# Performance work log

Measured on AMD Instinct MI355X. Metric: run time of the kernel, lower is better.

The kernel has to match this reference:

```python
import jax, jax.numpy as jnp
import numpy as np

N = 50000       # nodes
E = 800000      # edges (avg degree 16)
IN = 256        # input features
HEADS = 4
D = 32          # per-head dim (hidden_channels/heads = 128/4)
HID = HEADS * D # 128
OUT = 64        # out_channels, last layer has 1 head
SLOPE = 0.2     # DGL GATConv LeakyReLU negative slope


def setup_inputs() -> dict:
    key = jax.random.key(0)
    ks = jax.random.split(key, 11)
    s = 0.05
    return {
        "x": jax.random.normal(ks[0], (N, IN), jnp.float32),
        "W1": jax.random.normal(ks[1], (IN, HID), jnp.float32) * s,
        "al1": jax.random.normal(ks[2], (HEADS, D), jnp.float32) * s,
        "ar1": jax.random.normal(ks[3], (HEADS, D), jnp.float32) * s,
        "b1": jnp.zeros((HID,), jnp.float32),
        "W2": jax.random.normal(ks[4], (HID, OUT), jnp.float32) * s,
        "al2": jax.random.normal(ks[5], (1, OUT), jnp.float32) * s,
        "ar2": jax.random.normal(ks[6], (1, OUT), jnp.float32) * s,
        "b2": jnp.zeros((OUT,), jnp.float32),
        "src": jax.random.randint(ks[7], (E,), 0, N),
        "dst": jax.random.randint(ks[8], (E,), 0, N),
    }


def gat_conv(h, W, al, ar, b, src, dst, heads, d):
    # h: [N, F_in]; projects, computes edge attention, edge-softmax over dst,
    # scatter-reduce aggregation. Matches dglnn.GATConv (bias, no residual).
    feat = (h @ W).reshape(-1, heads, d)              # [N, H, D]
    el = jnp.einsum('nhd,hd->nh', feat, al)           # [N, H]
    er = jnp.einsum('nhd,hd->nh', feat, ar)           # [N, H]
    e = jax.nn.leaky_relu(el[src] + er[dst], SLOPE)   # [E, H] edge scores
    # edge softmax over incoming edges of each dst node
    m = jax.ops.segment_max(e, dst, num_segments=N)   # [N, H]
    ee = jnp.exp(e - m[dst])                          # [E, H]
    z = jax.ops.segment_sum(ee, dst, num_segments=N)  # [N, H]
    a = ee / z[dst]                                   # [E, H]
    msg = feat[src] * a[:, :, None]                   # [E, H, D] gather + weight
    out = jax.ops.segment_sum(msg, dst, num_segments=N)  # [N, H, D]
    return out + b.reshape(heads, d)


def reference(x, W1, al1, ar1, b1, W2, al2, ar2, b2, src, dst):
    h = gat_conv(x, W1, al1, ar1, b1, src, dst, HEADS, D)   # [N, 4, 32]
    h = jax.nn.relu(h).reshape(N, HID)                      # activation; dropout=identity (eval)
    h = gat_conv(h, W2, al2, ar2, b2, src, dst, 1, OUT)     # [N, 1, 64]
    return h.reshape(N, OUT)
```

## Files before the change

kernel.cpp:

```cpp
#include <hip/hip_runtime.h>
#include <math.h>

#define NN   50000
#define EE   800000
#define INF_ 256
#define HID  128
#define OUTF 64
#define DCAP 96
#define SLOPE 0.2f
#define G1B  782
#define NB   391
#define NCH  196
#define CHCAP 6144

typedef __attribute__((ext_vector_type(8))) short short8v;
typedef __attribute__((ext_vector_type(4))) float f32x4;

__device__ __forceinline__ float lrelu(float x) { return x > 0.f ? x : SLOPE * x; }
__device__ __forceinline__ float4 lrelu4(float4 v) {
  v.x = lrelu(v.x); v.y = lrelu(v.y); v.z = lrelu(v.z); v.w = lrelu(v.w); return v;
}
__device__ __forceinline__ unsigned short f2bf(float x) {
  unsigned int u = __float_as_uint(x);
  unsigned int r = (u + 0x7FFFu + ((u >> 16) & 1u)) >> 16;
  return (unsigned short)r;
}

__global__ __launch_bounds__(256) void prep_k(const int* __restrict__ src,
                                              const int* __restrict__ dst,
                                              int* __restrict__ cursor,
                                              int* __restrict__ packed,
                                              const float* __restrict__ W1,
                                              const float* __restrict__ W2,
                                              unsigned short* __restrict__ W1T,
                                              unsigned short* __restrict__ W2T) {
  int t = threadIdx.x;
  if (blockIdx.x >= NB) {
    int id = (blockIdx.x - NB) * 256 + t;
    if (id < 32768) {
      int k = id >> 7, c = id & 127;
      W1T[c * 256 + k] = f2bf(W1[k * 128 + c]);
    } else {
      int i2 = id - 32768;
      if (i2 < 8192) {
        int k = i2 >> 6, c = i2 & 63;
        W2T[c * 128 + k] = f2bf(W2[i2]);
      }
    }
    return;
  }
  __shared__ int h[NCH];
  __shared__ int cur[NCH];
  int b = blockIdx.x;
  if (t < NCH) h[t] = 0;
  __syncthreads();
  const int4* d4p = (const int4*)dst;
  const int4* s4p = (const int4*)src;
  int4 d4[2], s4[2];
  bool val[2];
#pragma unroll
  for (int it = 0; it < 2; ++it) {
    int qi = b * 512 + it * 256 + t;
    val[it] = qi < EE / 4;
    if (val[it]) {
      d4[it] = d4p[qi];
      s4[it] = s4p[qi];
      atomicAdd(&h[d4[it].x >> 8], 1);
      atomicAdd(&h[d4[it].y >> 8], 1);
      atomicAdd(&h[d4[it].z >> 8], 1);
      atomicAdd(&h[d4[it].w >> 8], 1);
    }
  }
  __syncthreads();
  if (t < NCH) {
    int c = h[t];
    cur[t] = t * CHCAP + ((c > 0) ? atomicAdd(&cursor[t], c) : 0);
  }
  __syncthreads();
#pragma unroll
  for (int it = 0; it < 2; ++it) {
    if (val[it]) {
      int p, c, lim;
      c = d4[it].x >> 8; lim = (c + 1) * CHCAP;
      p = atomicAdd(&cur[c], 1); if (p < lim) packed[p] = (s4[it].x << 8) | (d4[it].x & 255);
      c = d4[it].y >> 8; lim = (c + 1) * CHCAP;
      p = atomicAdd(&cur[c], 1); if (p < lim) packed[p] = (s4[it].y << 8) | (d4[it].y & 255);
      c = d4[it].z >> 8; lim = (c + 1) * CHCAP;
      p = atomicAdd(&cur[c], 1); if (p < lim) packed[p] = (s4[it].z << 8) | (d4[it].z & 255);
      c = d4[it].w >> 8; lim = (c + 1) * CHCAP;
      p = atomicAdd(&cur[c], 1); if (p < lim) packed[p] = (s4[it].w << 8) | (d4[it].w & 255);
    }
  }
}

__global__ __launch_bounds__(256) void cg1_k(const int* __restrict__ packed,
                                             const int* __restrict__ cursor,
                                             int* __restrict__ adj,
                                             int* __restrict__ rowptr,
                                             int* __restrict__ cnt,
                                             const float* __restrict__ x,
                                             const unsigned short* __restrict__ W1T,
                                             unsigned short* __restrict__ featb,
                                             const float* __restrict__ al,
                                             const float* __restrict__ ar,
                                             float* __restrict__ el,
                                             float* __restrict__ er) {
  __shared__ char smem[49152];
  int t = threadIdx.x;

  if (blockIdx.x < NCH) {
    int* pk  = (int*)smem;
    int* h   = (int*)(smem + 24576);
    int* sc  = (int*)(smem + 25600);
    int* cur = (int*)(smem + 26624);
    int b = blockIdx.x;
    int base = b * CHCAP;
    int len = cursor[b]; if (len > CHCAP) len = CHCAP;
    h[t] = 0;
    __syncthreads();
    for (int i = t; i < len; i += 256) {
      int v = packed[base + i];
      pk[i] = v;
      atomicAdd(&h[v & 255], 1);
    }
    __syncthreads();
    int v0 = h[t];
    sc[t] = v0;
    __syncthreads();
    for (int off = 1; off < 256; off <<= 1) {
      int add = (t >= off) ? sc[t - off] : 0;
      __syncthreads();
      sc[t] += add;
      __syncthreads();
    }
    int excl = sc[t] - v0;
    int node = b * 256 + t;
    if (node < NN) { cnt[node] = v0; rowptr[node] = base + excl; }
    cur[t] = excl;
    __syncthreads();
    for (int i = t; i < len; i += 256) {
      int v = pk[i];
      int p = atomicAdd(&cur[v & 255], 1);
      adj[base + p] = v & 0xFFFFFF00;
    }
    return;
  }

  unsigned short* As = (unsigned short*)smem;
  unsigned short* Bs = (unsigned short*)(smem + 16384);
  int lane = t & 63, wid = t >> 6;
  int n0 = (blockIdx.x - NCH) * 64;
  int wr = (wid >> 1) * 32;
  int wc = (wid & 1) * 64;

  f32x4 acc[2][4];
#pragma unroll
  for (int m = 0; m < 2; ++m)
#pragma unroll
    for (int n = 0; n < 4; ++n) acc[m][n] = (f32x4){0.f, 0.f, 0.f, 0.f};

  for (int pass = 0; pass < 2; ++pass) {
    int k0 = pass * 128;
#pragma unroll
    for (int it = 0; it < 8; ++it) {
      int f = it * 256 + t;
      int row = f >> 5;
      int c4  = f & 31;
      int grow = n0 + row;
      float4 v = make_float4(0.f, 0.f, 0.f, 0.f);
      if (grow < NN) v = *(const float4*)&x[grow * INF_ + k0 + c4 * 4];
      ushort4 b4;
      b4.x = f2bf(v.x); b4.y = f2bf(v.y); b4.z = f2bf(v.z); b4.w = f2bf(v.w);
      int byte = row * 256 + c4 * 8;
      byte ^= (row & 15) << 4;
      *(ushort4*)((char*)As + byte) = b4;
    }
#pragma unroll
    for (int it = 0; it < 8; ++it) {
      int f = it * 256 + t;
      int c  = f >> 4;
      int k8 = f & 15;
      uint4 v = *(const uint4*)&W1T[c * 256 + k0 + k8 * 8];
      int byte = c * 256 + k8 * 16;
      byte ^= (c & 15) << 4;
      *(uint4*)((char*)Bs + byte) = v;
    }
    __syncthreads();
#pragma unroll
    for (int ks = 0; ks < 4; ++ks) {
      int kb = ks * 64 + (lane >> 4) * 16;
      short8v a[2], b[4];
#pragma unroll
      for (int m = 0; m < 2; ++m) {
        int row = wr + m * 16 + (lane & 15);
        int byte = (row * 256 + kb) ^ ((row & 15) << 4);
        a[m] = *(const short8v*)((const char*)As + byte);
      }
#pragma unroll
      for (int n = 0; n < 4; ++n) {
        int c = wc + n * 16 + (lane & 15);
        int byte = (c * 256 + kb) ^ ((c & 15) << 4);
        b[n] = *(const short8v*)((const char*)Bs + byte);
      }
#pragma unroll
      for (int m = 0; m < 2; ++m)
#pragma unroll
        for (int n = 0; n < 4; ++n)
          acc[m][n] = __builtin_amdgcn_mfma_f32_16x16x32_bf16(a[m], b[n], acc[m][n], 0, 0, 0);
    }
    __syncthreads();
  }
#pragma unroll
  for (int m = 0; m < 2; ++m) {
    int rbase = wr + m * 16 + (lane >> 4) * 4;
#pragma unroll
    for (int r = 0; r < 4; ++r)
#pragma unroll
      for (int n = 0; n < 4; ++n)
        As[(rbase + r) * 128 + wc + n * 16 + (lane & 15)] = f2bf(acc[m][n][r]);
  }
  __syncthreads();
#pragma unroll
  for (int it = 0; it < 4; ++it) {
    int id = it * 256 + t;
    int row = id >> 4, c8 = id & 15;
    int grow = n0 + row;
    if (grow < NN)
      *(uint4*)&featb[grow * HID + c8 * 8] = *(const uint4*)&As[row * 128 + c8 * 8];
  }
  {
    int row = t >> 2, hh = t & 3;
    int grow = n0 + row;
    float pe = 0.f, pr = 0.f;
#pragma unroll
    for (int d = 0; d < 16; ++d) {
      unsigned int u = *(const unsigned int*)&As[row * 128 + hh * 32 + d * 2];
      float f0 = __uint_as_float(u << 16);
      float f1 = __uint_as_float(u & 0xFFFF0000u);
      float2 a2 = *(const float2*)&al[hh * 32 + d * 2];
      float2 r2 = *(const float2*)&ar[hh * 32 + d * 2];
      pe += f0 * a2.x + f1 * a2.y;
      pr += f0 * r2.x + f1 * r2.y;
    }
    if (grow < NN) { el[grow * 4 + hh] = pe; er[grow * 4 + hh] = pr; }
  }
}

__global__ __launch_bounds__(256) void agg1_k(const unsigned short* __restrict__ featb,
                                              const float* __restrict__ el1,
                                              const float* __restrict__ er1,
                                              const float* __restrict__ b1,
                                              const int* __restrict__ cnt,
                                              const int* __restrict__ rowptr,
                                              const int* __restrict__ adj,
                                              unsigned short* __restrict__ houtb) {
  __shared__ float ee[4][DCAP * 4];
  int wid = threadIdx.x >> 6, lane = threadIdx.x & 63;
  int n = blockIdx.x * 4 + wid;
  int deg = cnt[n]; if (deg > DCAP) deg = DCAP;
  const int* bk = adj + rowptr[n];
  float4 er = *(const float4*)(er1 + n * 4);
  int hl = lane >> 4;
  int m64 = deg < 64 ? deg : 64;
  int myoff = (lane < m64) ? bk[lane] : -1;
  const char* fb = (const char*)featb;
  int lb = lane * 4;

  float4 e4my = make_float4(0.f, 0.f, 0.f, 0.f);
  if (myoff >= 0 && deg <= 64)
    e4my = *(const float4*)((const char*)el1 + (myoff >> 4));
  unsigned int upre[16];
#pragma unroll
  for (int k = 0; k < 16; ++k) {
    int o = __shfl(myoff, k);
    upre[k] = *(const unsigned int*)(fb + ((k < m64) ? o : 0) + lb);
  }
  __builtin_amdgcn_sched_barrier(0);

  if (deg <= 64) {
    float4 ex = make_float4(0.f, 0.f, 0.f, 0.f);
    if (myoff >= 0) {
      float4 sc = lrelu4(make_float4(e4my.x + er.x, e4my.y + er.y,
                                     e4my.z + er.z, e4my.w + er.w));
      ex = make_float4(__expf(sc.x), __expf(sc.y), __expf(sc.z), __expf(sc.w));
    }
    float4 zs = ex;
#pragma unroll
    for (int off = 1; off < 64; off <<= 1) {
      zs.x += __shfl_xor(zs.x, off); zs.y += __shfl_xor(zs.y, off);
      zs.z += __shfl_xor(zs.z, off); zs.w += __shfl_xor(zs.w, off);
    }
    if (myoff >= 0) {
      float4 w = make_float4(ex.x / zs.x, ex.y / zs.y, ex.z / zs.z, ex.w / zs.w);
      *(float4*)&ee[wid][lane * 4] = w;
    }
  } else {
    float4 mx = make_float4(-INFINITY, -INFINITY, -INFINITY, -INFINITY);
    for (int j = lane; j < deg; j += 64) {
      int o = bk[j];
      float4 e4 = *(const float4*)((const char*)el1 + (o >> 4));
      float4 sc = lrelu4(make_float4(e4.x + er.x, e4.y + er.y, e4.z + er.z, e4.w + er.w));
      mx.x = fmaxf(mx.x, sc.x); mx.y = fmaxf(mx.y, sc.y);
      mx.z = fmaxf(mx.z, sc.z); mx.w = fmaxf(mx.w, sc.w);
    }
#pragma unroll
    for (int off = 1; off < 64; off <<= 1) {
      mx.x = fmaxf(mx.x, __shfl_xor(mx.x, off));
      mx.y = fmaxf(mx.y, __shfl_xor(mx.y, off));
      mx.z = fmaxf(mx.z, __shfl_xor(mx.z, off));
      mx.w = fmaxf(mx.w, __shfl_xor(mx.w, off));
    }
    float4 zs = make_float4(0.f, 0.f, 0.f, 0.f);
    for (int j = lane; j < deg; j += 64) {
      int o = bk[j];
      float4 e4 = *(const float4*)((const char*)el1 + (o >> 4));
      float4 sc = lrelu4(make_float4(e4.x + er.x, e4.y + er.y, e4.z + er.z, e4.w + er.w));
      float4 ex = make_float4(__expf(sc.x - mx.x), __expf(sc.y - mx.y),
                              __expf(sc.z - mx.z), __expf(sc.w - mx.w));
      *(float4*)&ee[wid][j * 4] = ex;
      zs.x += ex.x; zs.y += ex.y; zs.z += ex.z; zs.w += ex.w;
    }
#pragma unroll
    for (int off = 1; off < 64; off <<= 1) {
      zs.x += __shfl_xor(zs.x, off); zs.y += __shfl_xor(zs.y, off);
      zs.z += __shfl_xor(zs.z, off); zs.w += __shfl_xor(zs.w, off);
    }
    float4 iz = make_float4(1.f / zs.x, 1.f / zs.y, 1.f / zs.z, 1.f / zs.w);
    for (int j = lane; j < deg; j += 64) {
      float4 t = *(const float4*)&ee[wid][j * 4];
      t.x *= iz.x; t.y *= iz.y; t.z *= iz.z; t.w *= iz.w;
      *(float4*)&ee[wid][j * 4] = t;
    }
  }

  float acc0 = 0.f, acc1 = 0.f;
#pragma unroll
  for (int k = 0; k < 16; ++k) {
    float w = (k < m64) ? ee[wid][k * 4 + hl] : 0.f;
    acc0 += __uint_as_float(upre[k] << 16) * w;
    acc1 += __uint_as_float(upre[k] & 0xFFFF0000u) * w;
  }
  int j = 16;
  for (; j + 16 <= m64; j += 16) {
    unsigned int u[16];
#pragma unroll
    for (int q = 0; q < 16; ++q) {
      int o = __shfl(myoff, j + q);
      u[q] = *(const unsigned int*)(fb + o + lb);
    }
#pragma unroll
    for (int q = 0; q < 16; ++q) {
      float w = ee[wid][(j + q) * 4 + hl];
      acc0 += __uint_as_float(u[q] << 16) * w;
      acc1 += __uint_as_float(u[q] & 0xFFFF0000u) * w;
    }
  }
  for (; j + 4 <= m64; j += 4) {
    unsigned int u[4];
#pragma unroll
    for (int q = 0; q < 4; ++q) {
      int o = __shfl(myoff, j + q);
      u[q] = *(const unsigned int*)(fb + o + lb);
    }
#pragma unroll
    for (int q = 0; q < 4; ++q) {
      float w = ee[wid][(j + q) * 4 + hl];
      acc0 += __uint_as_float(u[q] << 16) * w;
      acc1 += __uint_as_float(u[q] & 0xFFFF0000u) * w;
    }
  }
  for (; j < m64; ++j) {
    int o = __shfl(myoff, j);
    unsigned int u = *(const unsigned int*)(fb + o + lb);
    float w = ee[wid][j * 4 + hl];
    acc0 += __uint_as_float(u << 16) * w; acc1 += __uint_as_float(u & 0xFFFF0000u) * w;
  }
  for (; j < deg; ++j) {
    int o = bk[j];
    unsigned int u = *(const unsigned int*)(fb + o + lb);
    float w = ee[wid][j * 4 + hl];
    acc0 += __uint_as_float(u << 16) * w; acc1 += __uint_as_float(u & 0xFFFF0000u) * w;
  }
  float2 bb = *(const float2*)&b1[lane * 2];
  float o0 = fmaxf(acc0 + bb.x, 0.f);
  float o1 = fmaxf(acc1 + bb.y, 0.f);
  unsigned int p = (unsigned int)f2bf(o0) | ((unsigned int)f2bf(o1) << 16);
  *(unsigned int*)&houtb[n * HID + lane * 2] = p;
}

__global__ __launch_bounds__(256) void gemm2s_mfma(const unsigned short* __restrict__ hb,
                                                   const unsigned short* __restrict__ W2T,
                                                   unsigned short* __restrict__ f2b,
                                                   const float* __restrict__ al2,
                                                   const float* __restrict__ ar2,
                                                   float* __restrict__ el2,
                                                   float* __restrict__ er2) {
  __shared__ char smem[32768];
  __shared__ float pel[64][4], per_[64][4];
  unsigned short* As = (unsigned short*)smem;
  unsigned short* Bs = (unsigned short*)(smem + 16384);
  int t = threadIdx.x, lane = t & 63, wid = t >> 6;
  int n0 = blockIdx.x * 64;
  f32x4 acc[4];
#pragma unroll
  for (int n = 0; n < 4; ++n) acc[n] = (f32x4){0.f, 0.f, 0.f, 0.f};

#pragma unroll
  for (int it = 0; it < 4; ++it) {
    int id = it * 256 + t;
    int row = id >> 4, c8 = id & 15;
    int grow = n0 + row;
    uint4 v = make_uint4(0, 0, 0, 0);
    if (grow < NN) v = *(const uint4*)&hb[grow * HID + c8 * 8];
    int byte = row * 256 + c8 * 16;
    byte ^= (row & 15) << 4;
    *(uint4*)((char*)As + byte) = v;
  }
#pragma unroll
  for (int it = 0; it < 4; ++it) {
    int id = it * 256 + t;
    int row = id >> 4, c8 = id & 15;
    uint4 v = *(const uint4*)&W2T[row * 128 + c8 * 8];
    int byte = row * 256 + c8 * 16;
    byte ^= (row & 15) << 4;
    *(uint4*)((char*)Bs + byte) = v;
  }
  __syncthreads();
  int wr = wid * 16;
#pragma unroll
  for (int ks = 0; ks < 4; ++ks) {
    int kb = ks * 64 + (lane >> 4) * 16;
    int arow = wr + (lane & 15);
    int abyte = (arow * 256 + kb) ^ ((arow & 15) << 4);
    short8v a = *(const short8v*)((const char*)As + abyte);
#pragma unroll
    for (int n = 0; n < 4; ++n) {
      int c = n * 16 + (lane & 15);
      int bbyte = (c * 256 + kb) ^ ((c & 15) << 4);
      short8v b = *(const short8v*)((const char*)Bs + bbyte);
      acc[n] = __builtin_amdgcn_mfma_f32_16x16x32_bf16(a, b, acc[n], 0, 0, 0);
    }
  }
  __syncthreads();
  float* stg = (float*)smem;
  unsigned short* sB = (unsigned short*)(smem + 16640);
  int rloc = wr + (lane >> 4) * 4;
#pragma unroll
  for (int r = 0; r < 4; ++r) {
#pragma unroll
    for (int n = 0; n < 4; ++n) {
      int col = n * 16 + (lane & 15);
      float v = acc[n][r];
      stg[(rloc + r) * 65 + col] = v;
      sB[(rloc + r) * 64 + col] = f2bf(v);
    }
  }
  __syncthreads();
#pragma unroll
  for (int it = 0; it < 2; ++it) {
    int id = it * 256 + t;
    int row = id >> 3, c8 = id & 7;
    int grow = n0 + row;
    if (grow < NN)
      *(uint4*)&f2b[grow * OUTF + c8 * 8] = *(const uint4*)&sB[row * 64 + c8 * 8];
  }
  {
    int row = t >> 2, seg = t & 3;
    float pe = 0.f, pr = 0.f;
#pragma unroll
    for (int d = 0; d < 16; ++d) {
      int c = seg * 16 + d;
      float f = stg[row * 65 + c];
      pe += f * al2[c];
      pr += f * ar2[c];
    }
    pel[row][seg] = pe; per_[row][seg] = pr;
  }
  __syncthreads();
  if (t < 64) {
    int grow = n0 + t;
    if (grow < NN) {
      el2[grow] = pel[t][0] + pel[t][1] + pel[t][2] + pel[t][3];
      er2[grow] = per_[t][0] + per_[t][1] + per_[t][2] + per_[t][3];
    }
  }
}

__global__ __launch_bounds__(256) void agg2_k(const unsigned short* __restrict__ f2b,
                                              const float* __restrict__ el2,
                                              const float* __restrict__ er2,
                                              const float* __restrict__ b2,
                                              const int* __restrict__ cnt,
                                              const int* __restrict__ rowptr,
                                              const int* __restrict__ adj,
                                              float* __restrict__ out) {
  __shared__ float ee[4][DCAP];
  int wid = threadIdx.x >> 6, lane = threadIdx.x & 63;
  int n = blockIdx.x * 4 + wid;
  int deg = cnt[n]; if (deg > DCAP) deg = DCAP;
  const int* bk = adj + rowptr[n];
  float er = er2[n];
  int m64 = deg < 64 ? deg : 64;
  int myoff = (lane < m64) ? bk[lane] : -1;
  int half = lane >> 5, c2 = (lane & 31) * 2;
  const char* fb = (const char*)f2b;

  float elmy = 0.f;
  if (myoff >= 0 && deg <= 64)
    elmy = *(const float*)((const char*)el2 + (myoff >> 6));
  unsigned int upre[8];
#pragma unroll
  for (int s = 0; s < 8; ++s) {
    int je = s * 2 + half;
    int o = __shfl(myoff, je);
    upre[s] = *(const unsigned int*)(fb + ((je < m64) ? (o >> 1) : 0) + c2 * 2);
  }
  __builtin_amdgcn_sched_barrier(0);

  if (deg <= 64) {
    float ex = (myoff >= 0) ? __expf(lrelu(elmy + er)) : 0.f;
    float zs = ex;
#pragma unroll
    for (int off = 1; off < 64; off <<= 1) zs += __shfl_xor(zs, off);
    if (myoff >= 0) ee[wid][lane] = ex / zs;
  } else {
    float mx = -INFINITY;
    for (int j = lane; j < deg; j += 64) {
      int o = bk[j];
      mx = fmaxf(mx, lrelu(*(const float*)((const char*)el2 + (o >> 6)) + er));
    }
#pragma unroll
    for (int off = 1; off < 64; off <<= 1) mx = fmaxf(mx, __shfl_xor(mx, off));
    float zs = 0.f;
    for (int j = lane; j < deg; j += 64) {
      int o = bk[j];
      float ex = __expf(lrelu(*(const float*)((const char*)el2 + (o >> 6)) + er) - mx);
      ee[wid][j] = ex;
      zs += ex;
    }
#pragma unroll
    for (int off = 1; off < 64; off <<= 1) zs += __shfl_xor(zs, off);
    float iz = 1.f / zs;
    for (int j = lane; j < deg; j += 64) ee[wid][j] *= iz;
  }

  float acc0 = 0.f, acc1 = 0.f;
#pragma unroll
  for (int s = 0; s < 8; ++s) {
    int je = s * 2 + half;
    float w = (je < m64) ? ee[wid][je] : 0.f;
    acc0 += __uint_as_float(upre[s] << 16) * w;
    acc1 += __uint_as_float(upre[s] & 0xFFFF0000u) * w;
  }
  int j = 16;
  for (; j + 16 <= deg; j += 16) {
    unsigned int u[8]; float w[8];
#pragma unroll
    for (int q = 0; q < 8; ++q) {
      int je = j + q * 2 + half;
      int os = __shfl(myoff, je < 64 ? je : 63);
      int o = (je < 64) ? os : bk[je];
      u[q] = *(const unsigned int*)(fb + (o >> 1) + c2 * 2);
      w[q] = ee[wid][je];
    }
#pragma unroll
    for (int q = 0; q < 8; ++q) {
      acc0 += __uint_as_float(u[q] << 16) * w[q];
      acc1 += __uint_as_float(u[q] & 0xFFFF0000u) * w[q];
    }
  }
  for (; j < deg; j += 2) {
    int je = j + half;
    int os = __shfl(myoff, (je < 64) ? je : 63);
    float w = 0.f; unsigned int u = 0;
    if (je < deg) {
      int o = (je < 64) ? os : bk[je];
      u = *(const unsigned int*)(fb + (o >> 1) + c2 * 2);
      w = ee[wid][je];
    }
    acc0 += __uint_as_float(u << 16) * w;
    acc1 += __uint_as_float(u & 0xFFFF0000u) * w;
  }
  acc0 += __shfl_xor(acc0, 32);
  acc1 += __shfl_xor(acc1, 32);
  if (lane < 32) {
    float2 bb = *(const float2*)&b2[c2];
    *(float2*)&out[n * OUTF + c2] = make_float2(acc0 + bb.x, acc1 + bb.y);
  }
}

extern "C" void kernel_launch(void* const* d_in, const int* in_sizes, int n_in,
                              void* d_out, int out_size, void* d_ws, size_t ws_size,
                              hipStream_t stream) {
  const float* x   = (const float*)d_in[0];
  const float* W1  = (const float*)d_in[1];
  const float* al1 = (const float*)d_in[2];
  const float* ar1 = (const float*)d_in[3];
  const float* b1  = (const float*)d_in[4];
  const float* W2  = (const float*)d_in[5];
  const float* al2 = (const float*)d_in[6];
  const float* ar2 = (const float*)d_in[7];
  const float* b2  = (const float*)d_in[8];
  const int*   src = (const int*)d_in[9];
  const int*   dst = (const int*)d_in[10];
  float* out = (float*)d_out;

  char* base = (char*)d_ws;
  unsigned short* feat1b = (unsigned short*)base;
  unsigned short* f2b    = (unsigned short*)base;
  unsigned short* hb     = (unsigned short*)(base + 12800000);
  float* el1 = (float*)(base + 25600000);
  float* er1 = el1 + NN * 4;
  float* el2 = er1 + NN * 4;
  float* er2 = el2 + NN;
  int* cnt    = (int*)(er2 + NN);
  int* rowptr = cnt + NN;
  int* adj    = rowptr + NN;
  int* packed = adj + NCH * CHCAP;
  int* cursor = packed + NCH * CHCAP;
  unsigned short* W1T = (unsigned short*)(cursor + NCH);
  unsigned short* W2T = W1T + 256 * 128;

  hipMemsetAsync(cursor, 0, NCH * sizeof(int), stream);
  prep_k <<<NB + 161, 256, 0, stream>>>(src, dst, cursor, packed, W1, W2, W1T, W2T);
  cg1_k  <<<NCH + G1B, 256, 0, stream>>>(packed, cursor, adj, rowptr, cnt,
                                         x, W1T, feat1b, al1, ar1, el1, er1);
  agg1_k <<<NN / 4, 256, 0, stream>>>(feat1b, el1, er1, b1, cnt, rowptr, adj, hb);
  gemm2s_mfma<<<G1B, 256, 0, stream>>>(hb, W2T, f2b, al2, ar2, el2, er2);
  agg2_k <<<NN / 4, 256, 0, stream>>>(f2b, el2, er2, b2, cnt, rowptr, adj, out);
}
```

Baseline: 115.4 us.

## Halve GEMM shared memory by staging W1 in two column chunks

Shared memory in the fused CSR-build/GEMM kernel drops from 48KB to 32KB by loading the W1 tile in two 64-column halves instead of all 128 columns at once. Each wave now owns 16 rows and all columns, iterating over two column chunks with extra barriers. The goal is higher occupancy (more blocks per CU). The cost is more synchronisation and repeated A-fragment reads. Per-wave MFMA count is unchanged.

Result: no change. 115.5 us (+0.1%).

```diff
diff --git a/kernel.cpp b/kernel.cpp
--- a/kernel.cpp
+++ b/kernel.cpp
@@ -105,7 +105,7 @@
                                              const float* __restrict__ ar,
                                              float* __restrict__ el,
                                              float* __restrict__ er) {
-  __shared__ char smem[49152];
+  __shared__ char smem[32768];
   int t = threadIdx.x;
 
   if (blockIdx.x < NCH) {
@@ -150,8 +150,7 @@
   unsigned short* Bs = (unsigned short*)(smem + 16384);
   int lane = t & 63, wid = t >> 6;
   int n0 = (blockIdx.x - NCH) * 64;
-  int wr = (wid >> 1) * 32;
-  int wc = (wid & 1) * 64;
+  int wr = wid * 16;
 
   f32x4 acc[2][4];
 #pragma unroll
@@ -176,48 +175,43 @@
       *(ushort4*)((char*)As + byte) = b4;
     }
 #pragma unroll
-    for (int it = 0; it < 8; ++it) {
-      int f = it * 256 + t;
-      int c  = f >> 4;
-      int k8 = f & 15;
-      uint4 v = *(const uint4*)&W1T[c * 256 + k0 + k8 * 8];
-      int byte = c * 256 + k8 * 16;
-      byte ^= (c & 15) << 4;
-      *(uint4*)((char*)Bs + byte) = v;
-    }
-    __syncthreads();
-#pragma unroll
-    for (int ks = 0; ks < 4; ++ks) {
-      int kb = ks * 64 + (lane >> 4) * 16;
-      short8v a[2], b[4];
-#pragma unroll
-      for (int m = 0; m < 2; ++m) {
-        int row = wr + m * 16 + (lane & 15);
-        int byte = (row * 256 + kb) ^ ((row & 15) << 4);
-        a[m] = *(const short8v*)((const char*)As + byte);
+    for (int ch = 0; ch < 2; ++ch) {
+#pragma unroll
+      for (int it = 0; it < 4; ++it) {
+        int f = it * 256 + t;
+        int c  = f >> 4;
+        int k8 = f & 15;
+        uint4 v = *(const uint4*)&W1T[(ch * 64 + c) * 256 + k0 + k8 * 8];
+        int byte = c * 256 + k8 * 16;
+        byte ^= (c & 15) << 4;
+        *(uint4*)((char*)Bs + byte) = v;
       }
-#pragma unroll
-      for (int n = 0; n < 4; ++n) {
-        int c = wc + n * 16 + (lane & 15);
-        int byte = (c * 256 + kb) ^ ((c & 15) << 4);
-        b[n] = *(const short8v*)((const char*)Bs + byte);
+      __syncthreads();
+#pragma unroll
+      for (int ks = 0; ks < 4; ++ks) {
+        int kb = ks * 64 + (lane >> 4) * 16;
+        int arow = wr + (lane & 15);
+        int abyte = (arow * 256 + kb) ^ ((arow & 15) << 4);
+        short8v a = *(const short8v*)((const char*)As + abyte);
+#pragma unroll
+        for (int n = 0; n < 4; ++n) {
+          int c = n * 16 + (lane & 15);
+          int bbyte = (c * 256 + kb) ^ ((c & 15) << 4);
+          short8v b = *(const short8v*)((const char*)Bs + bbyte);
+          acc[ch][n] = __builtin_amdgcn_mfma_f32_16x16x32_bf16(a, b, acc[ch][n], 0, 0, 0);
+        }
       }
-#pragma unroll
-      for (int m = 0; m < 2; ++m)
-#pragma unroll
-        for (int n = 0; n < 4; ++n)
-          acc[m][n] = __builtin_amdgcn_mfma_f32_16x16x32_bf16(a[m], b[n], acc[m][n], 0, 0, 0);
-    }
-    __syncthreads();
-  }
-#pragma unroll
-  for (int m = 0; m < 2; ++m) {
-    int rbase = wr + m * 16 + (lane >> 4) * 4;
+      __syncthreads();
+    }
+  }
+#pragma unroll
+  for (int ch = 0; ch < 2; ++ch) {
+    int rbase = wr + (lane >> 4) * 4;
 #pragma unroll
     for (int r = 0; r < 4; ++r)
 #pragma unroll
       for (int n = 0; n < 4; ++n)
-        As[(rbase + r) * 128 + wc + n * 16 + (lane & 15)] = f2bf(acc[m][n][r]);
+        As[(rbase + r) * 128 + ch * 64 + n * 16 + (lane & 15)] = f2bf(acc[ch][n][r]);
   }
   __syncthreads();
 #pragma unroll
```
